# Kernel optimization log

Measured on AMD Instinct MI355X. Metric: run time of the kernel, lower is better.

Reference implementation:

```python
import jax, jax.numpy as jnp
import numpy as np

B, N, IN_C, HID, K1, K2, OUT_C = 128, 512, 128, 32, 100, 10, 10
E_PER = 8192  # edges per graph (avg degree 16)
EPS = 1e-15


def _lin(key, fan_in, fan_out):
    return jax.random.normal(key, (fan_in, fan_out), jnp.float32) / np.sqrt(fan_in)


def setup_inputs() -> dict:
    key = jax.random.key(0)
    ks = jax.random.split(key, 20)
    total = B * N
    x = jax.random.normal(ks[0], (total, IN_C), jnp.float32)
    # per-graph random edges, offset into the global node index space
    src_l = jax.random.randint(ks[1], (B, E_PER), 0, N)
    dst_l = jax.random.randint(ks[2], (B, E_PER), 0, N)
    off = (jnp.arange(B, dtype=jnp.int32) * N)[:, None]
    edge_index = jnp.stack([(src_l + off).reshape(-1), (dst_l + off).reshape(-1)]).astype(jnp.int32)
    batch = (jnp.arange(total, dtype=jnp.int32) // N).astype(jnp.int32)
    return {
        "x": x,
        "edge_index": edge_index,
        "batch": batch,
        "conv1_W": _lin(ks[3], IN_C, HID), "conv1_b": jnp.zeros((HID,), jnp.float32),
        "pool1_W": _lin(ks[4], HID, K1), "pool1_b": jnp.zeros((K1,), jnp.float32),
        "conv2_rel_W": _lin(ks[5], HID, HID), "conv2_rel_b": jnp.zeros((HID,), jnp.float32),
        "conv2_root_W": _lin(ks[6], HID, HID),
        "pool2_W": _lin(ks[7], HID, K2), "pool2_b": jnp.zeros((K2,), jnp.float32),
        "conv3_rel_W": _lin(ks[8], HID, HID), "conv3_rel_b": jnp.zeros((HID,), jnp.float32),
        "conv3_root_W": _lin(ks[9], HID, HID),
        "lin1_W": _lin(ks[10], HID, HID), "lin1_b": jnp.zeros((HID,), jnp.float32),
        "lin2_W": _lin(ks[11], HID, OUT_C), "lin2_b": jnp.zeros((OUT_C,), jnp.float32),
    }


def gcn_conv(x, edge_index, W, b):
    # GCNConv with add_self_loops=True, symmetric normalization
    total = x.shape[0]
    loops = jnp.arange(total, dtype=edge_index.dtype)
    src = jnp.concatenate([edge_index[0], loops])
    dst = jnp.concatenate([edge_index[1], loops])
    w = jnp.ones(src.shape[0], x.dtype)
    deg = jax.ops.segment_sum(w, dst, num_segments=total)
    dis = jnp.where(deg > 0, jax.lax.rsqrt(deg), 0.0)
    norm = dis[src] * dis[dst]
    xw = x @ W
    out = jax.ops.segment_sum(norm[:, None] * xw[src], dst, num_segments=total)
    return out + b


def dense_mincut_pool(x, adj, s, mask=None):
    # x:[b,n,f] adj:[b,n,n] s:[b,n,k]
    s = jax.nn.softmax(s, axis=-1)
    if mask is not None:
        m = mask[..., None].astype(x.dtype)
        x = x * m
        s = s * m
    out = jnp.einsum('bnk,bnf->bkf', s, x)
    out_adj = jnp.einsum('bnk,bnm,bml->bkl', s, adj, s)
    mincut_num = jnp.trace(out_adj, axis1=-2, axis2=-1)
    d_flat = adj.sum(-1)  # [b,n]
    mincut_den = jnp.einsum('bnk,bn,bnk->b', s, d_flat, s)  # trace(s^T D s)
    mincut_loss = jnp.mean(-(mincut_num / mincut_den))
    k = s.shape[-1]
    ss = jnp.einsum('bnk,bnl->bkl', s, s)
    ss_norm = jnp.linalg.norm(ss, axis=(-1, -2), keepdims=True)
    i_s = jnp.eye(k, dtype=x.dtype) / jnp.sqrt(jnp.asarray(k, x.dtype))  # I_k / ||I_k||_F
    ortho_loss = jnp.mean(jnp.linalg.norm(ss / ss_norm - i_s, axis=(-1, -2)))
    # zero diagonal then symmetric degree-normalize
    out_adj = out_adj * (1.0 - jnp.eye(k, dtype=x.dtype))
    d = jnp.sqrt(out_adj.sum(-1))[..., None] + EPS
    out_adj = out_adj / d / jnp.swapaxes(d, -1, -2)
    return out, out_adj, mincut_loss, ortho_loss


def dense_graph_conv(x, adj, rel_W, rel_b, root_W):
    # DenseGraphConv(aggr='add'): lin_rel(adj @ x) + lin_root(x)
    return (adj @ x) @ rel_W + rel_b + x @ root_W


def reference(x, edge_index, batch, conv1_W, conv1_b, pool1_W, pool1_b,
              conv2_rel_W, conv2_rel_b, conv2_root_W, pool2_W, pool2_b,
              conv3_rel_W, conv3_rel_b, conv3_root_W, lin1_W, lin1_b, lin2_W, lin2_b):
    h = jax.nn.relu(gcn_conv(x, edge_index, conv1_W, conv1_b))
    # to_dense_batch: sorted batch with N nodes per graph -> reshape; mask all-true
    xd = h.reshape(B, N, HID)
    mask = jnp.ones((B, N), bool)
    # to_dense_adj
    b_idx = edge_index[0] // N
    s_l = edge_index[0] % N
    d_l = edge_index[1] % N
    adj = jnp.zeros((B, N, N), x.dtype).at[b_idx, s_l, d_l].add(1.0)
    s = xd @ pool1_W + pool1_b
    xd, adj, mc1, o1 = dense_mincut_pool(xd, adj, s, mask)
    xd = jax.nn.relu(dense_graph_conv(xd, adj, conv2_rel_W, conv2_rel_b, conv2_root_W))
    s = xd @ pool2_W + pool2_b
    xd, adj, mc2, o2 = dense_mincut_pool(xd, adj, s)
    xd = dense_graph_conv(xd, adj, conv3_rel_W, conv3_rel_b, conv3_root_W)
    g = xd.mean(axis=1)  # [B, HID]
    g = jax.nn.relu(g @ lin1_W + lin1_b)
    g = g @ lin2_W + lin2_b
    return jax.nn.log_softmax(g, axis=-1), mc1 + mc2 + o1 + o2
```

## Files before the change

### kernel.cpp

```cpp
#include <hip/hip_runtime.h>
#include <hip/hip_bf16.h>

#define TB   128
#define NN   512
#define INC  128
#define HH   32
#define KP1  100
#define KP2  10
#define OC   10
#define EPER 8192
#define NT   (TB*NN)
#define ET   (TB*EPER)
#define ZTR  264
#define ZTS  40
#define XTS  136

typedef unsigned int  u32;
typedef unsigned short u16;
typedef __attribute__((ext_vector_type(8))) short bf16x8;
typedef __attribute__((ext_vector_type(16))) float f32x16;

__device__ __forceinline__ u32 bfr(float f) {
    u32 b = __float_as_uint(f);
    return (b + 0x7fffu + ((b >> 16) & 1u)) >> 16;
}
__device__ __forceinline__ u32 pk2(float a, float b) { return bfr(a) | (bfr(b) << 16); }
__device__ __forceinline__ float blo(u32 u) { return __uint_as_float(u << 16); }
__device__ __forceinline__ float bhi(u32 u) { return __uint_as_float(u & 0xffff0000u); }

__global__ void k_init(float* __restrict__ aux) {
    int i = blockIdx.x * 256 + threadIdx.x;
    if (i < 1024) aux[i] = 0.0f;
}

__global__ __launch_bounds__(1024) void k_sort(const int* __restrict__ ei,
                                               int* __restrict__ cnt_src, int* __restrict__ cnt_dst,
                                               int* __restrict__ off_src, int* __restrict__ off_dst,
                                               u16* __restrict__ srt_dst, u16* __restrict__ srt_src,
                                               float* __restrict__ dis) {
    __shared__ int hs[NN], hd[NN], ps[NN], pd[NN];
    __shared__ __align__(16) u16 sdl[EPER], ssl[EPER];
    int g = blockIdx.x, tid = threadIdx.x, goff = g * NN;
    if (tid < NN) { hs[tid] = 0; hd[tid] = 0; }
    __syncthreads();
    const int* es = ei + (size_t)g * EPER;
    const int* ed = ei + ET + (size_t)g * EPER;
    for (int e = tid; e < EPER; e += 1024) {
        atomicAdd(&hs[es[e] - goff], 1);
        atomicAdd(&hd[ed[e] - goff], 1);
    }
    __syncthreads();
    int vs = 0, vd = 0;
    if (tid < NN) { vs = hs[tid]; vd = hd[tid]; ps[tid] = vs; pd[tid] = vd; }
    __syncthreads();
    for (int off = 1; off < NN; off <<= 1) {
        int xa = 0, xb = 0;
        if (tid < NN) {
            xa = ps[tid]; xb = pd[tid];
            if (tid >= off) { xa += ps[tid - off]; xb += pd[tid - off]; }
        }
        __syncthreads();
        if (tid < NN) { ps[tid] = xa; pd[tid] = xb; }
        __syncthreads();
    }
    int eso = 0, edo = 0;
    if (tid < NN) {
        eso = ps[tid] - vs; edo = pd[tid] - vd;
        cnt_src[goff + tid] = vs;  cnt_dst[goff + tid] = vd;
        off_src[goff + tid] = g * EPER + eso;
        off_dst[goff + tid] = g * EPER + edo;
        dis[goff + tid] = rsqrtf(1.0f + (float)vd);
    }
    __syncthreads();
    if (tid < NN) { ps[tid] = eso; pd[tid] = edo; }
    __syncthreads();
    for (int e = tid; e < EPER; e += 1024) {
        int s = es[e] - goff, d = ed[e] - goff;
        int p = atomicAdd(&ps[s], 1); sdl[p] = (u16)d;
        int q = atomicAdd(&pd[d], 1); ssl[q] = (u16)s;
    }
    __syncthreads();
    u32* wd = (u32*)(srt_dst + (size_t)g * EPER);
    u32* ws = (u32*)(srt_src + (size_t)g * EPER);
    const u32* rd = (const u32*)sdl;
    const u32* rs = (const u32*)ssl;
    for (int i = tid; i < EPER / 2; i += 1024) { wd[i] = rd[i]; ws[i] = rs[i]; }
}

__global__ __launch_bounds__(256) void k_xw2(const float* __restrict__ x, const float* __restrict__ W,
                                             u16* __restrict__ xwb) {
    __shared__ u16 sX[128 * XTS];
    __shared__ u16 sW[32 * XTS];
    int tid = threadIdx.x;
    int nbase = blockIdx.x * 128;
    for (int i = tid; i < INC * HH; i += 256) {
        int k = i >> 5, n = i & 31;
        sW[n * XTS + k] = (u16)bfr(W[i]);
    }
    for (int i = tid; i < 128 * 32; i += 256) {
        int r = i >> 5, q = i & 31;
        float4 v = ((const float4*)(x + (size_t)(nbase + r) * INC))[q];
        u32* dst = (u32*)&sX[r * XTS + q * 4];
        dst[0] = pk2(v.x, v.y);
        dst[1] = pk2(v.z, v.w);
    }
    __syncthreads();
    int wave = tid >> 6, lane = tid & 63;
    int lc = lane & 31, half = lane >> 5;
    f32x16 acc;
#pragma unroll
    for (int r = 0; r < 16; r++) acc[r] = 0.f;
#pragma unroll
    for (int kc = 0; kc < 8; kc++) {
        bf16x8 af  = *(const bf16x8*)&sX[(wave * 32 + lc) * XTS + kc * 16 + half * 8];
        bf16x8 bfv = *(const bf16x8*)&sW[lc * XTS + kc * 16 + half * 8];
        acc = __builtin_amdgcn_mfma_f32_32x32x16_bf16(af, bfv, acc, 0, 0, 0);
    }
#pragma unroll
    for (int r = 0; r < 16; r++) {
        int m = (r & 3) + 8 * (r >> 2) + 4 * half;
        int rowg = nbase + wave * 32 + m;
        xwb[(size_t)rowg * HH + lc] = (u16)bfr(acc[r]);
    }
}

__global__ __launch_bounds__(256) void k_gcng(const u16* __restrict__ ssrc, const int* __restrict__ od,
                                              const int* __restrict__ cd, const u32* __restrict__ xwb32,
                                              const float* __restrict__ dis, const float* __restrict__ bias,
                                              u32* __restrict__ hb32) {
    int tid = threadIdx.x;
    int b = blockIdx.x;
    int r8 = b & 7, j = b >> 3;
    int g = r8 + 8 * (j & 15);
    int chunk = j >> 4;
    int n = g * NN + chunk * 16 + (tid >> 4), cp = tid & 15;
    int goff = g * NN;
    int base = od[n], cnt = cd[n];
    float dn = dis[n];
    u32 us = xwb32[(size_t)n * 16 + cp];
    float a0 = dn * blo(us), a1 = dn * bhi(us);
    int i = 0;
    for (; i + 4 <= cnt; i += 4) {
        int s0 = goff + ssrc[base + i],     s1v = goff + ssrc[base + i + 1];
        int s2 = goff + ssrc[base + i + 2], s3  = goff + ssrc[base + i + 3];
        float d0 = dis[s0], d1 = dis[s1v], d2 = dis[s2], d3 = dis[s3];
        u32 u0 = xwb32[(size_t)s0 * 16 + cp];
        u32 u1 = xwb32[(size_t)s1v * 16 + cp];
        u32 u2 = xwb32[(size_t)s2 * 16 + cp];
        u32 u3 = xwb32[(size_t)s3 * 16 + cp];
        a0 += d0 * blo(u0) + d1 * blo(u1) + d2 * blo(u2) + d3 * blo(u3);
        a1 += d0 * bhi(u0) + d1 * bhi(u1) + d2 * bhi(u2) + d3 * bhi(u3);
    }
    for (; i < cnt; i++) {
        int s0 = goff + ssrc[base + i]; float d0 = dis[s0];
        u32 u0 = xwb32[(size_t)s0 * 16 + cp];
        a0 += d0 * blo(u0); a1 += d0 * bhi(u0);
    }
    float v0 = fmaxf(dn * a0 + bias[2 * cp], 0.f);
    float v1 = fmaxf(dn * a1 + bias[2 * cp + 1], 0.f);
    hb32[(size_t)n * 16 + cp] = pk2(v0, v1);
}

__global__ __launch_bounds__(256) void k_s1m(const u32* __restrict__ hb32, const float* __restrict__ W,
                                             const float* __restrict__ bias, const int* __restrict__ csrc,
                                             u16* __restrict__ s1b, float* __restrict__ den1) {
    __shared__ u16 sH[128 * ZTS];
    __shared__ u16 sW[128 * ZTS];
    int tid = threadIdx.x;
    int nbase = blockIdx.x * 128;
    for (int i = tid; i < HH * KP1; i += 256) {
        int k = i / KP1, n = i - k * KP1;
        sW[n * ZTS + k] = (u16)bfr(W[i]);
    }
    for (int i = tid; i < 28 * 16; i += 256) {
        int n = 100 + (i >> 4), q = i & 15;
        ((u32*)sW)[n * (ZTS / 2) + q] = 0;
    }
    for (int i = tid; i < 128 * 16; i += 256) {
        int r = i >> 4, q = i & 15;
        ((u32*)sH)[r * (ZTS / 2) + q] = hb32[(size_t)(nbase + r) * 16 + q];
    }
    __syncthreads();
    int wave = tid >> 6, lane = tid & 63;
    int lc = lane & 31, half = lane >> 5;
    f32x16 acc[4];
#pragma unroll
    for (int t = 0; t < 4; t++)
#pragma unroll
        for (int r = 0; r < 16; r++) acc[t][r] = 0.f;
#pragma unroll
    for (int kc = 0; kc < 2; kc++) {
        bf16x8 af = *(const bf16x8*)&sH[(wave * 32 + lc) * ZTS + kc * 16 + half * 8];
#pragma unroll
        for (int t = 0; t < 4; t++) {
            bf16x8 bfv = *(const bf16x8*)&sW[(t * 32 + lc) * ZTS + kc * 16 + half * 8];
            acc[t] = __builtin_amdgcn_mfma_f32_32x32x16_bf16(af, bfv, acc[t], 0, 0, 0);
        }
    }
    float s[16], q[16];
#pragma unroll
    for (int r = 0; r < 16; r++) { s[r] = 0.f; q[r] = 0.f; }
#pragma unroll
    for (int t = 0; t < 4; t++) {
        int ch = t * 32 + lc;
        bool valid = ch < KP1;
        float bv = valid ? bias[ch] : 0.f;
#pragma unroll
        for (int r = 0; r < 16; r++) {
            float ev = valid ? __expf(acc[t][r] + bv) : 0.f;
            acc[t][r] = ev; s[r] += ev; q[r] = fmaf(ev, ev, q[r]);
        }
    }
#pragma unroll
    for (int off = 16; off >= 1; off >>= 1) {
#pragma unroll
        for (int r = 0; r < 16; r++) { s[r] += __shfl_xor(s[r], off); q[r] += __shfl_xor(q[r], off); }
    }
    float inv[16];
#pragma unroll
    for (int r = 0; r < 16; r++) inv[r] = 1.f / s[r];
#pragma unroll
    for (int t = 0; t < 4; t++) {
        int ch = t * 32 + lc;
        if (ch < KP1) {
#pragma unroll
            for (int r = 0; r < 16; r++) {
                int lr = (r & 3) + 8 * (r >> 2) + 4 * half;
                int rowg = nbase + wave * 32 + lr;
                s1b[(size_t)rowg * KP1 + ch] = (u16)bfr(acc[t][r] * inv[r]);
            }
        }
    }
    float contrib = 0.f;
    if (lc == 0) {
#pragma unroll
        for (int r = 0; r < 16; r++) {
            int lr = (r & 3) + 8 * (r >> 2) + 4 * half;
            int rowg = nbase + wave * 32 + lr;
            contrib += (float)csrc[rowg] * q[r] * inv[r] * inv[r];
        }
    }
    contrib += __shfl_xor(contrib, 32);
    if (lane == 0) atomicAdd(&den1[nbase >> 9], contrib);
}

__global__ __launch_bounds__(256) void k_t1g(const u16* __restrict__ sdst, const int* __restrict__ osr,
                                             const int* __restrict__ csr, const u32* __restrict__ s1b32,
                                             u32* __restrict__ t1b32) {
    int tid = threadIdx.x;
    int b = blockIdx.x;
    int r8 = b & 7, j = b >> 3;
    int g = r8 + 8 * (j & 15);
    int chunk = j >> 4;
    int n = g * NN + chunk * 4 + (tid >> 6), lane = tid & 63;
    if (lane >= 50) return;
    int goff = g * NN;
    int base = osr[n], cnt = csr[n];
    float a0 = 0.f, a1 = 0.f;
    int i = 0;
    for (; i + 4 <= cnt; i += 4) {
        int d0 = goff + sdst[base + i],     d1 = goff + sdst[base + i + 1];
        int d2 = goff + sdst[base + i + 2], d3 = goff + sdst[base + i + 3];
        u32 u0 = s1b32[(size_t)d0 * 50 + lane];
        u32 u1 = s1b32[(size_t)d1 * 50 + lane];
        u32 u2 = s1b32[(size_t)d2 * 50 + lane];
        u32 u3 = s1b32[(size_t)d3 * 50 + lane];
        a0 += (blo(u0) + blo(u1)) + (blo(u2) + blo(u3));
        a1 += (bhi(u0) + bhi(u1)) + (bhi(u2) + bhi(u3));
    }
    for (; i < cnt; i++) {
        int d0 = goff + sdst[base + i];
        u32 u0 = s1b32[(size_t)d0 * 50 + lane];
        a0 += blo(u0); a1 += bhi(u0);
    }
    t1b32[(size_t)n * 50 + lane] = pk2(a0, a1);
}

__global__ __launch_bounds__(512, 2) void k_gram(const u32* __restrict__ s1b32, const u32* __restrict__ t1b32,
                                                 const u32* __restrict__ hb32,
                                                 float* __restrict__ A1n, float* __restrict__ P1,
                                                 float* __restrict__ aux) {
    __shared__ u16 sZ[2][ZTR * ZTS];
    __shared__ float sC[KP1 * 232];
    __shared__ float sRow[KP1], sd[KP1];
    __shared__ float sScal[3];
    int g = blockIdx.x;
    int nbase = g * NN;
    int tid = threadIdx.x;
    int wave = tid >> 6, lane = tid & 63;
    int mt = wave & 3;
    int nt0 = (wave >> 2) * 4;
    int lc = lane & 31, half = lane >> 5;

    f32x16 acc[4];
#pragma unroll
    for (int t = 0; t < 4; t++)
#pragma unroll
        for (int r = 0; r < 16; r++) acc[t][r] = 0.f;

    if (tid < KP1) sRow[tid] = 0.f;
    if (tid < 3) sScal[tid] = 0.f;
    for (int i = tid; i < 32 * ZTS; i += 512) {
        int r = 232 + i / ZTS, c = i % ZTS;
        sZ[0][r * ZTS + c] = 0; sZ[1][r * ZTS + c] = 0;
    }
#pragma unroll
    for (int j = 0; j < 4; j++) {
        int i = tid + j * 512;
        if (i < 32 * 58) {
            int r = i / 58, q = i - r * 58;
            int n = nbase + r;
            uint2 v; int ch0;
            if (q < 25)      { v = ((const uint2*)(t1b32 + (size_t)n * 50))[q];      ch0 = 4 * q; }
            else if (q < 33) { v = ((const uint2*)(hb32  + (size_t)n * 16))[q - 25]; ch0 = 100 + 4 * (q - 25); }
            else             { v = ((const uint2*)(s1b32 + (size_t)n * 50))[q - 33]; ch0 = 132 + 4 * (q - 33); }
            sZ[0][(ch0    ) * ZTS + r] = (u16)(v.x & 0xffffu);
            sZ[0][(ch0 + 1) * ZTS + r] = (u16)(v.x >> 16);
            sZ[0][(ch0 + 2) * ZTS + r] = (u16)(v.y & 0xffffu);
            sZ[0][(ch0 + 3) * ZTS + r] = (u16)(v.y >> 16);
        }
    }
    __syncthreads();

    for (int nt = 0; nt < 16; nt++) {
        uint2 pre[4];
        if (nt < 15) {
#pragma unroll
            for (int j = 0; j < 4; j++) {
                int i = tid + j * 512;
                if (i < 32 * 58) {
                    int r = i / 58, q = i - r * 58;
                    int n = nbase + (nt + 1) * 32 + r;
                    uint2 v;
                    if (q < 25)      v = ((const uint2*)(t1b32 + (size_t)n * 50))[q];
                    else if (q < 33) v = ((const uint2*)(hb32  + (size_t)n * 16))[q - 25];
                    else             v = ((const uint2*)(s1b32 + (size_t)n * 50))[q - 33];
                    pre[j] = v;
                }
            }
        }
        const u16* zb = sZ[nt & 1];
#pragma unroll
        for (int mf = 0; mf < 2; mf++) {
            bf16x8 af = *(const bf16x8*)&zb[(132 + mt * 32 + lc) * ZTS + mf * 16 + half * 8];
#pragma unroll
            for (int t = 0; t < 4; t++) {
                bf16x8 bfv = *(const bf16x8*)&zb[((nt0 + t) * 32 + lc) * ZTS + mf * 16 + half * 8];
                acc[t] = __builtin_amdgcn_mfma_f32_32x32x16_bf16(af, bfv, acc[t], 0, 0, 0);
            }
        }
        if (nt < 15) {
            u16* zo = sZ[(nt + 1) & 1];
#pragma unroll
            for (int j = 0; j < 4; j++) {
                int i = tid + j * 512;
                if (i < 32 * 58) {
                    int r = i / 58, q = i - r * 58;
                    int ch0 = (q < 25) ? (4 * q) : ((q < 33) ? (100 + 4 * (q - 25)) : (132 + 4 * (q - 33)));
                    zo[(ch0    ) * ZTS + r] = (u16)(pre[j].x & 0xffffu);
                    zo[(ch0 + 1) * ZTS + r] = (u16)(pre[j].x >> 16);
                    zo[(ch0 + 2) * ZTS + r] = (u16)(pre[j].y & 0xffffu);
                    zo[(ch0 + 3) * ZTS + r] = (u16)(pre[j].y >> 16);
                }
            }
        }
        __syncthreads();
    }
#pragma unroll
    for (int t = 0; t < 4; t++) {
        int l = (nt0 + t) * 32 + lc;
        if (l < 232) {
#pragma unroll
            for (int r = 0; r < 16; r++) {
                int k = mt * 32 + (r & 3) + 8 * (r >> 2) + 4 * half;
                if (k < KP1) sC[k * 232 + l] = acc[t][r];
            }
        }
    }
    __syncthreads();
    float ssq = 0.f, trss = 0.f, troa = 0.f;
    for (int idx = tid; idx < KP1 * 58; idx += 512) {
        int k = idx / 58, q = idx - k * 58;
        float4 s = *(const float4*)&sC[k * 232 + q * 4];
        int c = q * 4;
        if (c < 100) {
            float rs = (s.x + s.y) + (s.z + s.w);
            if (k >= c && k < c + 4) { float d = ((const float*)&s)[k - c]; troa += d; rs -= d; }
            atomicAdd(&sRow[k], rs);
        } else if (c < 132) {
            *(float4*)&P1[((size_t)g * KP1 + k) * HH + (c - 100)] = s;
        } else {
            ssq += s.x * s.x + s.y * s.y + s.z * s.z + s.w * s.w;
            int l0 = c - 132;
            if (k >= l0 && k < l0 + 4) trss += ((const float*)&s)[k - l0];
        }
    }
#pragma unroll
    for (int off = 32; off >= 1; off >>= 1) {
        ssq  += __shfl_xor(ssq, off);
        trss += __shfl_xor(trss, off);
        troa += __shfl_xor(troa, off);
    }
    if ((tid & 63) == 0) {
        atomicAdd(&sScal[0], troa);
        atomicAdd(&sScal[1], trss);
        atomicAdd(&sScal[2], ssq);
    }
    __syncthreads();
    if (tid == 0) {
        float o1 = sqrtf(fmaxf(2.f - 2.f * sScal[1] / (sqrtf(sScal[2]) * 10.f), 0.f));
        aux[128 + g] = -(sScal[0] / aux[g]) + o1;
    }
    if (tid < KP1) sd[tid] = sqrtf(sRow[tid]) + 1e-15f;
    __syncthreads();
    for (int i = tid; i < KP1 * KP1; i += 512) {
        int k = i / KP1, l = i - k * KP1;
        A1n[(size_t)g * (KP1 * KP1) + i] = (k == l) ? 0.f : sC[k * 232 + l] / (sd[k] * sd[l]);
    }
}

__global__ __launch_bounds__(512) void k_s2a(const float* __restrict__ A1n, const float* __restrict__ P1,
                                             const float* __restrict__ relW, const float* __restrict__ relB,
                                             const float* __restrict__ rootW,
                                             const float* __restrict__ p2W, const float* __restrict__ p2B,
                                             float* __restrict__ P2, float* __restrict__ A2n,
                                             float* __restrict__ aux) {
    __shared__ float sX[KP1 * HH];
    __shared__ float sY[KP1 * HH];
    __shared__ float sS2[KP1 * KP2];
    __shared__ float sT2[KP1 * KP2];
    __shared__ float sA2[100], sB2[100], sdd[10], red[100];
    int g = blockIdx.x, tid = threadIdx.x;
    const float* Ag = A1n + (size_t)g * (KP1 * KP1);
    for (int i = tid; i < KP1 * HH; i += 512) sX[i] = P1[(size_t)g * (KP1 * HH) + i];
    __syncthreads();

    int n = tid >> 2, cq = tid & 3;
    if (tid < 400) {
        float yv[8];
#pragma unroll
        for (int j = 0; j < 8; j++) yv[j] = 0.f;
        for (int mq = 0; mq < 25; mq++) {
            float4 a4 = *(const float4*)&Ag[n * KP1 + mq * 4];
            const float* xb = &sX[(mq * 4) * HH + cq * 8];
            float aa[4] = {a4.x, a4.y, a4.z, a4.w};
#pragma unroll
            for (int mm = 0; mm < 4; mm++) {
                const float* xr = xb + mm * HH;
#pragma unroll
                for (int j = 0; j < 8; j++) yv[j] = fmaf(aa[mm], xr[j], yv[j]);
            }
        }
#pragma unroll
        for (int j = 0; j < 8; j++) sY[n * HH + cq * 8 + j] = yv[j];
    }
    __syncthreads();
    float x2v[8];
    if (tid < 400) {
#pragma unroll
        for (int j = 0; j < 8; j++) x2v[j] = relB[cq * 8 + j];
        for (int j = 0; j < 32; j++) {
            float yj = sY[n * HH + j];
            float xj = sX[n * HH + j];
            float4 r0 = *(const float4*)&relW[j * 32 + cq * 8];
            float4 r1v = *(const float4*)&relW[j * 32 + cq * 8 + 4];
            float4 q0 = *(const float4*)&rootW[j * 32 + cq * 8];
            float4 q1 = *(const float4*)&rootW[j * 32 + cq * 8 + 4];
            x2v[0] += yj * r0.x + xj * q0.x;  x2v[1] += yj * r0.y + xj * q0.y;
            x2v[2] += yj * r0.z + xj * q0.z;  x2v[3] += yj * r0.w + xj * q0.w;
            x2v[4] += yj * r1v.x + xj * q1.x; x2v[5] += yj * r1v.y + xj * q1.y;
            x2v[6] += yj * r1v.z + xj * q1.z; x2v[7] += yj * r1v.w + xj * q1.w;
        }
    }
    __syncthreads();
    if (tid < 400) {
#pragma unroll
        for (int j = 0; j < 8; j++) sX[n * HH + cq * 8 + j] = fmaxf(x2v[j], 0.f);
    }
    __syncthreads();
    if (tid < KP1) {
        float lg[10];
#pragma unroll
        for (int j = 0; j < 10; j++) lg[j] = p2B[j];
        for (int c = 0; c < 32; c++) {
            float xv = sX[tid * HH + c];
#pragma unroll
            for (int j = 0; j < 10; j++) lg[j] = fmaf(xv, p2W[c * 10 + j], lg[j]);
        }
        float mx = lg[0];
#pragma unroll
        for (int j = 1; j < 10; j++) mx = fmaxf(mx, lg[j]);
        float se = 0.f;
#pragma unroll
        for (int j = 0; j < 10; j++) { lg[j] = __expf(lg[j] - mx); se += lg[j]; }
        float inv = 1.f / se, sq = 0.f;
#pragma unroll
        for (int j = 0; j < 10; j++) { float sv = lg[j] * inv; sS2[tid * 10 + j] = sv; sq += sv * sv; }
        float d2 = 0.f;
        for (int mq = 0; mq < 25; mq++) {
            float4 a4 = *(const float4*)&Ag[tid * KP1 + mq * 4];
            d2 += a4.x + a4.y + a4.z + a4.w;
        }
        red[tid] = d2 * sq;
    }
    __syncthreads();
    for (int p = tid; p < KP1 * KP2; p += 512) {
        int n2 = p / 10, jj = p % 10;
        float a = 0.f;
        for (int m = 0; m < KP1; m++) a = fmaf(Ag[n2 * KP1 + m], sS2[m * 10 + jj], a);
        sT2[p] = a;
    }
    if (tid < KP2 * HH) {
        int k = tid >> 5, cc = tid & 31;
        float a = 0.f;
        for (int n2 = 0; n2 < KP1; n2++) a = fmaf(sS2[n2 * 10 + k], sX[n2 * HH + cc], a);
        P2[(size_t)g * (KP2 * HH) + tid] = a;
    }
    __syncthreads();
    if (tid < 100) {
        int k = tid / 10, l = tid % 10;
        float oa = 0.f, ss = 0.f;
        for (int n2 = 0; n2 < KP1; n2++) {
            float sk = sS2[n2 * 10 + k];
            oa = fmaf(sk, sT2[n2 * 10 + l], oa);
            ss = fmaf(sk, sS2[n2 * 10 + l], ss);
        }
        sA2[tid] = oa; sB2[tid] = ss;
    }
    __syncthreads();
    if (tid == 0) {
        float den2 = 0.f;
        for (int i = 0; i < 100; i++) den2 += red[i];
        float troa = 0.f, trss = 0.f, ssq = 0.f;
        for (int k = 0; k < 10; k++) { troa += sA2[k * 10 + k]; trss += sB2[k * 10 + k]; }
        for (int i = 0; i < 100; i++) ssq += sB2[i] * sB2[i];
        float o2 = sqrtf(fmaxf(2.f - 2.f * trss / (sqrtf(ssq) * 3.16227766f), 0.f));
        aux[256 + g] = -(troa / den2) + o2;
    }
    if (tid < 10) {
        float rs = 0.f;
        for (int l = 0; l < 10; l++) if (l != tid) rs += sA2[tid * 10 + l];
        sdd[tid] = sqrtf(rs) + 1e-15f;
    }
    __syncthreads();
    if (tid < 100) {
        int k = tid / 10, l = tid % 10;
        A2n[(size_t)g * 100 + tid] = (k == l) ? 0.f : sA2[tid] / (sdd[k] * sdd[l]);
    }
}

__global__ __launch_bounds__(64) void k_s2b(const float* __restrict__ P2, const float* __restrict__ A2n,
                                            const float* __restrict__ relW3, const float* __restrict__ relb3,
                                            const float* __restrict__ rootW3,
                                            const float* __restrict__ l1W, const float* __restrict__ l1b,
                                            const float* __restrict__ l2W, const float* __restrict__ l2b,
                                            float* __restrict__ out) {
    __shared__ float sP[KP2 * HH], sA2[100], sY3[KP2 * HH], sG[32], sG1[32], sL[10], sLse;
    int g = blockIdx.x, tid = threadIdx.x;
    for (int i = tid; i < KP2 * HH; i += 64) sP[i] = P2[(size_t)g * (KP2 * HH) + i];
    for (int i = tid; i < 100; i += 64) sA2[i] = A2n[(size_t)g * 100 + i];
    if (tid < 32) sG[tid] = 0.f;
    __syncthreads();
    for (int p = tid; p < KP2 * HH; p += 64) {
        int k = p >> 5, cc = p & 31;
        float a = 0.f;
#pragma unroll
        for (int m = 0; m < 10; m++) a = fmaf(sA2[k * 10 + m], sP[m * HH + cc], a);
        sY3[p] = a;
    }
    __syncthreads();
    for (int p = tid; p < KP2 * HH; p += 64) {
        int k = p >> 5, cc = p & 31;
        float v = relb3[cc];
        for (int j = 0; j < 32; j++)
            v += sY3[k * HH + j] * relW3[j * 32 + cc] + sP[k * HH + j] * rootW3[j * 32 + cc];
        atomicAdd(&sG[cc], v * 0.1f);
    }
    __syncthreads();
    if (tid < 32) {
        float v = l1b[tid];
        for (int j = 0; j < 32; j++) v = fmaf(sG[j], l1W[j * 32 + tid], v);
        sG1[tid] = fmaxf(v, 0.f);
    }
    __syncthreads();
    if (tid < 10) {
        float v = l2b[tid];
        for (int j = 0; j < 32; j++) v = fmaf(sG1[j], l2W[j * 10 + tid], v);
        sL[tid] = v;
    }
    __syncthreads();
    if (tid == 0) {
        float mx = sL[0];
        for (int j = 1; j < 10; j++) mx = fmaxf(mx, sL[j]);
        float se = 0.f;
        for (int j = 0; j < 10; j++) se += expf(sL[j] - mx);
        sLse = mx + logf(se);
    }
    __syncthreads();
    if (tid < 10) out[(size_t)g * 10 + tid] = sL[tid] - sLse;
}

__global__ void k_loss(const float* __restrict__ aux, float* __restrict__ out) {
    __shared__ float red[128];
    int tid = threadIdx.x;
    red[tid] = aux[128 + tid] + aux[256 + tid];
    __syncthreads();
#pragma unroll
    for (int s = 64; s > 0; s >>= 1) { if (tid < s) red[tid] += red[tid + s]; __syncthreads(); }
    if (tid == 0) out[1280] = red[0] * (1.f / 128.f);
}

extern "C" void kernel_launch(void* const* d_in, const int* in_sizes, int n_in,
                              void* d_out, int out_size, void* d_ws, size_t ws_size,
                              hipStream_t stream) {
    const float* x    = (const float*)d_in[0];
    const int*   ei   = (const int*)d_in[1];
    const float* c1W  = (const float*)d_in[3];
    const float* c1b  = (const float*)d_in[4];
    const float* p1W  = (const float*)d_in[5];
    const float* p1b  = (const float*)d_in[6];
    const float* relW2  = (const float*)d_in[7];
    const float* relb2  = (const float*)d_in[8];
    const float* rootW2 = (const float*)d_in[9];
    const float* p2W  = (const float*)d_in[10];
    const float* p2b  = (const float*)d_in[11];
    const float* relW3  = (const float*)d_in[12];
    const float* relb3  = (const float*)d_in[13];
    const float* rootW3 = (const float*)d_in[14];
    const float* l1W  = (const float*)d_in[15];
    const float* l1b  = (const float*)d_in[16];
    const float* l2W  = (const float*)d_in[17];
    const float* l2b  = (const float*)d_in[18];
    float* out = (float*)d_out;

    int*  cnt_src = (int*)d_ws;
    int*  cnt_dst = cnt_src + NT;
    int*  off_src = cnt_dst + NT;
    int*  off_dst = off_src + NT;
    u16*  srt_dst = (u16*)(off_dst + NT);
    u16*  srt_src = srt_dst + ET;
    float* dis = (float*)(srt_src + ET);
    u32*  xwb  = (u32*)(dis + NT);
    u32*  hb   = xwb + (size_t)NT * 16;
    u32*  s1b  = hb + (size_t)NT * 16;
    u32*  t1b  = s1b + (size_t)NT * 50;
    float* A1n  = (float*)(t1b + (size_t)NT * 50);
    float* P1   = A1n + (size_t)TB * KP1 * KP1;
    float* P2   = P1 + (size_t)TB * KP1 * HH;
    float* A2n  = P2 + (size_t)TB * KP2 * HH;
    float* aux  = A2n + (size_t)TB * 100;

    k_init<<<4, 256, 0, stream>>>(aux);
    k_sort<<<TB, 1024, 0, stream>>>(ei, cnt_src, cnt_dst, off_src, off_dst, srt_dst, srt_src, dis);
    k_xw2<<<NT / 128, 256, 0, stream>>>(x, c1W, (u16*)xwb);
    k_gcng<<<NT / 16, 256, 0, stream>>>(srt_src, off_dst, cnt_dst, xwb, dis, c1b, hb);
    k_s1m<<<NT / 128, 256, 0, stream>>>(hb, p1W, p1b, cnt_src, (u16*)s1b, aux );
    k_t1g<<<NT / 4, 256, 0, stream>>>(srt_dst, off_src, cnt_src, s1b, t1b);
    k_gram<<<TB, 512, 0, stream>>>(s1b, t1b, hb, A1n, P1, aux);
    k_s2a<<<TB, 512, 0, stream>>>(A1n, P1, relW2, relb2, rootW2, p2W, p2b, P2, A2n, aux);
    k_s2b<<<TB, 64, 0, stream>>>(P2, A2n, relW3, relb3, rootW3, l1W, l1b, l2W, l2b, out);
    k_loss<<<1, 128, 0, stream>>>(aux, out);
}
```

Measured before the change: 286.9 us.

## Double k_gram block to 1024 threads and pack LDS tile stores per 4 nodes

k_gram now runs 16 waves per graph, with each wave owning two 32-column output tiles instead of four, which halves the per-wave MFMA chain and the accumulator register count. The staging of the transposed Z tile is rewritten so each work item loads one u32 from four consecutive nodes and writes four bf16 values as a single 8-byte LDS store. The previous scheme wrote scattered 16-bit stores. The goal is more latency hiding in a grid of only 128 blocks and lower LDS store overhead, at the cost of strided global loads and heavier barrier synchronisation across 16 waves.

```diff
diff --git a/kernel.cpp b/kernel.cpp
--- a/kernel.cpp
+++ b/kernel.cpp
@@ -276,11 +276,37 @@
     t1b32[(size_t)n * 50 + lane] = pk2(a0, a1);
 }
 
-__global__ __launch_bounds__(512, 2) void k_gram(const u32* __restrict__ s1b32, const u32* __restrict__ t1b32,
-                                                 const u32* __restrict__ hb32,
-                                                 float* __restrict__ A1n, float* __restrict__ P1,
-                                                 float* __restrict__ aux) {
-    __shared__ u16 sZ[2][ZTR * ZTS];
+__device__ __forceinline__ void ld_item(int i, int nodebase,
+                                        const u32* __restrict__ t1, const u32* __restrict__ h,
+                                        const u32* __restrict__ s1,
+                                        u32& w0, u32& w1, u32& w2, u32& w3) {
+    int ch = i >> 3, rq = i & 7;
+    int n0 = nodebase + rq * 4;
+    if (ch < 100) {
+        const u32* p = t1 + (size_t)n0 * 50 + (ch >> 1);
+        w0 = p[0]; w1 = p[50]; w2 = p[100]; w3 = p[150];
+    } else if (ch < 132) {
+        const u32* p = h + (size_t)n0 * 16 + ((ch - 100) >> 1);
+        w0 = p[0]; w1 = p[16]; w2 = p[32]; w3 = p[48];
+    } else {
+        const u32* p = s1 + (size_t)n0 * 50 + ((ch - 132) >> 1);
+        w0 = p[0]; w1 = p[50]; w2 = p[100]; w3 = p[150];
+    }
+}
+__device__ __forceinline__ void st_item(u16* __restrict__ zb, int i,
+                                        u32 w0, u32 w1, u32 w2, u32 w3) {
+    int ch = i >> 3, rq = i & 7;
+    u32 sh = (u32)(ch & 1) * 16u;
+    u32 e0 = (w0 >> sh) & 0xffffu, e1 = (w1 >> sh) & 0xffffu;
+    u32 e2 = (w2 >> sh) & 0xffffu, e3 = (w3 >> sh) & 0xffffu;
+    *(uint2*)&zb[ch * ZTS + rq * 4] = make_uint2(e0 | (e1 << 16), e2 | (e3 << 16));
+}
+
+__global__ __launch_bounds__(1024, 1) void k_gram(const u32* __restrict__ s1b32, const u32* __restrict__ t1b32,
+                                                  const u32* __restrict__ hb32,
+                                                  float* __restrict__ A1n, float* __restrict__ P1,
+                                                  float* __restrict__ aux) {
+    __shared__ __align__(16) u16 sZ[2][ZTR * ZTS];
     __shared__ float sC[KP1 * 232];
     __shared__ float sRow[KP1], sd[KP1];
     __shared__ float sScal[3];
@@ -289,97 +315,71 @@
     int tid = threadIdx.x;
     int wave = tid >> 6, lane = tid & 63;
     int mt = wave & 3;
-    int nt0 = (wave >> 2) * 4;
+    int ct = wave >> 2;
     int lc = lane & 31, half = lane >> 5;
 
-    f32x16 acc[4];
-#pragma unroll
-    for (int t = 0; t < 4; t++)
-#pragma unroll
-        for (int r = 0; r < 16; r++) acc[t][r] = 0.f;
+    f32x16 acc0, acc1;
+#pragma unroll
+    for (int r = 0; r < 16; r++) { acc0[r] = 0.f; acc1[r] = 0.f; }
 
     if (tid < KP1) sRow[tid] = 0.f;
     if (tid < 3) sScal[tid] = 0.f;
-    for (int i = tid; i < 32 * ZTS; i += 512) {
+    for (int i = tid; i < 32 * ZTS; i += 1024) {
         int r = 232 + i / ZTS, c = i % ZTS;
         sZ[0][r * ZTS + c] = 0; sZ[1][r * ZTS + c] = 0;
     }
-#pragma unroll
-    for (int j = 0; j < 4; j++) {
-        int i = tid + j * 512;
-        if (i < 32 * 58) {
-            int r = i / 58, q = i - r * 58;
-            int n = nbase + r;
-            uint2 v; int ch0;
-            if (q < 25)      { v = ((const uint2*)(t1b32 + (size_t)n * 50))[q];      ch0 = 4 * q; }
-            else if (q < 33) { v = ((const uint2*)(hb32  + (size_t)n * 16))[q - 25]; ch0 = 100 + 4 * (q - 25); }
-            else             { v = ((const uint2*)(s1b32 + (size_t)n * 50))[q - 33]; ch0 = 132 + 4 * (q - 33); }
-            sZ[0][(ch0    ) * ZTS + r] = (u16)(v.x & 0xffffu);
-            sZ[0][(ch0 + 1) * ZTS + r] = (u16)(v.x >> 16);
-            sZ[0][(ch0 + 2) * ZTS + r] = (u16)(v.y & 0xffffu);
-            sZ[0][(ch0 + 3) * ZTS + r] = (u16)(v.y >> 16);
-        }
+    for (int i = tid; i < 232 * 8; i += 1024) {
+        u32 w0, w1, w2, w3;
+        ld_item(i, nbase, t1b32, hb32, s1b32, w0, w1, w2, w3);
+        st_item(sZ[0], i, w0, w1, w2, w3);
     }
     __syncthreads();
 
     for (int nt = 0; nt < 16; nt++) {
-        uint2 pre[4];
+        u32 a0w, a1w, a2w, a3w, b0w, b1w, b2w, b3w;
+        int ia = tid, ib = tid + 1024;
         if (nt < 15) {
-#pragma unroll
-            for (int j = 0; j < 4; j++) {
-                int i = tid + j * 512;
-                if (i < 32 * 58) {
-                    int r = i / 58, q = i - r * 58;
-                    int n = nbase + (nt + 1) * 32 + r;
-                    uint2 v;
-                    if (q < 25)      v = ((const uint2*)(t1b32 + (size_t)n * 50))[q];
-                    else if (q < 33) v = ((const uint2*)(hb32  + (size_t)n * 16))[q - 25];
-                    else             v = ((const uint2*)(s1b32 + (size_t)n * 50))[q - 33];
-                    pre[j] = v;
-                }
-            }
+            int nb2 = nbase + (nt + 1) * 32;
+            ld_item(ia, nb2, t1b32, hb32, s1b32, a0w, a1w, a2w, a3w);
+            if (ib < 232 * 8) ld_item(ib, nb2, t1b32, hb32, s1b32, b0w, b1w, b2w, b3w);
         }
         const u16* zb = sZ[nt & 1];
 #pragma unroll
         for (int mf = 0; mf < 2; mf++) {
             bf16x8 af = *(const bf16x8*)&zb[(132 + mt * 32 + lc) * ZTS + mf * 16 + half * 8];
-#pragma unroll
-            for (int t = 0; t < 4; t++) {
-                bf16x8 bfv = *(const bf16x8*)&zb[((nt0 + t) * 32 + lc) * ZTS + mf * 16 + half * 8];
-                acc[t] = __builtin_amdgcn_mfma_f32_32x32x16_bf16(af, bfv, acc[t], 0, 0, 0);
-            }
+            bf16x8 bv0 = *(const bf16x8*)&zb[((ct * 2    ) * 32 + lc) * ZTS + mf * 16 + half * 8];
+            bf16x8 bv1 = *(const bf16x8*)&zb[((ct * 2 + 1) * 32 + lc) * ZTS + mf * 16 + half * 8];
+            acc0 = __builtin_amdgcn_mfma_f32_32x32x16_bf16(af, bv0, acc0, 0, 0, 0);
+            acc1 = __builtin_amdgcn_mfma_f32_32x32x16_bf16(af, bv1, acc1, 0, 0, 0);
         }
         if (nt < 15) {
             u16* zo = sZ[(nt + 1) & 1];
-#pragma unroll
-            for (int j = 0; j < 4; j++) {
-                int i = tid + j * 512;
-                if (i < 32 * 58) {
-                    int r = i / 58, q = i - r * 58;
-                    int ch0 = (q < 25) ? (4 * q) : ((q < 33) ? (100 + 4 * (q - 25)) : (132 + 4 * (q - 33)));
-                    zo[(ch0    ) * ZTS + r] = (u16)(pre[j].x & 0xffffu);
-                    zo[(ch0 + 1) * ZTS + r] = (u16)(pre[j].x >> 16);
-                    zo[(ch0 + 2) * ZTS + r] = (u16)(pre[j].y & 0xffffu);
-                    zo[(ch0 + 3) * ZTS + r] = (u16)(pre[j].y >> 16);
-                }
-            }
+            st_item(zo, ia, a0w, a1w, a2w, a3w);
+            if (ib < 232 * 8) st_item(zo, ib, b0w, b1w, b2w, b3w);
         }
         __syncthreads();
     }
-#pragma unroll
-    for (int t = 0; t < 4; t++) {
-        int l = (nt0 + t) * 32 + lc;
-        if (l < 232) {
+    {
+        int l0 = (ct * 2) * 32 + lc;
+        if (l0 < 232) {
 #pragma unroll
             for (int r = 0; r < 16; r++) {
                 int k = mt * 32 + (r & 3) + 8 * (r >> 2) + 4 * half;
-                if (k < KP1) sC[k * 232 + l] = acc[t][r];
+                if (k < KP1) sC[k * 232 + l0] = acc0[r];
             }
         }
+        int l1 = (ct * 2 + 1) * 32 + lc;
+        if (l1 < 232) {
+#pragma unroll
+            for (int r = 0; r < 16; r++) {
+                int k = mt * 32 + (r & 3) + 8 * (r >> 2) + 4 * half;
+                if (k < KP1) sC[k * 232 + l1] = acc1[r];
+            }
+        }
     }
     __syncthreads();
     float ssq = 0.f, trss = 0.f, troa = 0.f;
-    for (int idx = tid; idx < KP1 * 58; idx += 512) {
+    for (int idx = tid; idx < KP1 * 58; idx += 1024) {
         int k = idx / 58, q = idx - k * 58;
         float4 s = *(const float4*)&sC[k * 232 + q * 4];
         int c = q * 4;
@@ -413,7 +413,7 @@
     }
     if (tid < KP1) sd[tid] = sqrtf(sRow[tid]) + 1e-15f;
     __syncthreads();
-    for (int i = tid; i < KP1 * KP1; i += 512) {
+    for (int i = tid; i < KP1 * KP1; i += 1024) {
         int k = i / KP1, l = i - k * KP1;
         A1n[(size_t)g * (KP1 * KP1) + i] = (k == l) ? 0.f : sC[k * 232 + l] / (sd[k] * sd[l]);
     }
@@ -656,7 +656,7 @@
     k_gcng<<<NT / 16, 256, 0, stream>>>(srt_src, off_dst, cnt_dst, xwb, dis, c1b, hb);
     k_s1m<<<NT / 128, 256, 0, stream>>>(hb, p1W, p1b, cnt_src, (u16*)s1b, aux );
     k_t1g<<<NT / 4, 256, 0, stream>>>(srt_dst, off_src, cnt_src, s1b, t1b);
-    k_gram<<<TB, 512, 0, stream>>>(s1b, t1b, hb, A1n, P1, aux);
+    k_gram<<<TB, 1024, 0, stream>>>(s1b, t1b, hb, A1n, P1, aux);
     k_s2a<<<TB, 512, 0, stream>>>(A1n, P1, relW2, relb2, rootW2, p2W, p2b, P2, A2n, aux);
     k_s2b<<<TB, 64, 0, stream>>>(P2, A2n, relW3, relb3, rootW3, l1W, l1b, l2W, l2b, out);
     k_loss<<<1, 128, 0, stream>>>(aux, out);
```

After: 295.2 us. 2.9% more time.
